# Kernel optimization log

Hardware: AMD Instinct MI355X
Metric: run time of the kernel (lower is better)

## Reference

```python
import jax, jax.numpy as jnp
import numpy as np

B, S, H = 64, 4096, 512

def setup_inputs() -> dict:
    key = jax.random.key(0)
    ks = jax.random.split(key, 8)
    decoder_output = jax.random.normal(ks[0], (B, H), dtype=jnp.float32)
    encoder_output = jax.random.normal(ks[1], (B, S, 2 * H), dtype=jnp.float32)
    mask = jax.random.randint(ks[2], (B, S), 0, 2).astype(bool)
    mask = mask.at[:, 0].set(True)  # guarantee at least one valid position per row
    sc_h = 1.0 / np.sqrt(2 * H)
    sc_s = 1.0 / np.sqrt(H)
    W_h_w = jax.random.uniform(ks[3], (H, 2 * H), jnp.float32, -sc_h, sc_h)
    W_h_b = jax.random.uniform(ks[4], (H,), jnp.float32, -sc_h, sc_h)
    W_s_w = jax.random.uniform(ks[5], (H, H), jnp.float32, -sc_s, sc_s)
    W_s_b = jax.random.uniform(ks[6], (H,), jnp.float32, -sc_s, sc_s)
    v_w = jax.random.uniform(ks[7], (1, H), jnp.float32, -sc_s, sc_s)
    return {"decoder_output": decoder_output, "encoder_output": encoder_output,
            "mask": mask, "W_h_w": W_h_w, "W_h_b": W_h_b,
            "W_s_w": W_s_w, "W_s_b": W_s_b, "v_w": v_w}

def reference(decoder_output, encoder_output, mask, W_h_w, W_h_b, W_s_w, W_s_b, v_w):
    # enc proj: [B,S,H]; dec proj: [B,H] broadcast over S
    enc = jnp.einsum('bse,he->bsh', encoder_output, W_h_w) + W_h_b
    dec = decoder_output @ W_s_w.T + W_s_b  # [B,H]
    x = jnp.tanh(enc + dec[:, None, :])     # [B,S,H]
    scores = jnp.einsum('bsh,h->bs', x, v_w[0])  # [B,S]
    masked = jnp.where(mask, scores, -jnp.inf)
    return jax.nn.softmax(masked, axis=-1)
```

## Files before the change

### kernel.cpp

```cpp
#include <hip/hip_runtime.h>
#include <math.h>

typedef __attribute__((ext_vector_type(8))) short bf16x8;
typedef __attribute__((ext_vector_type(4))) float f32x4;
typedef __attribute__((ext_vector_type(4))) unsigned short u16x4;

#define NB 64
#define NS 4096
#define NH 512
#define NE 1024
#define APITCH 80

__device__ __forceinline__ unsigned short f2bf(float f) {
  unsigned int u = __float_as_uint(f);
  u += 0x7fffu + ((u >> 16) & 1u);
  return (unsigned short)(u >> 16);
}

__device__ __forceinline__ float fast_tanh(float x) {
  float e = __expf(2.0f * x);
  return 1.0f - 2.0f * __builtin_amdgcn_rcpf(e + 1.0f);
}

__global__ __launch_bounds__(256) void prep_b_kernel(const float* __restrict__ W,
                                                     unsigned short* __restrict__ Bp) {
  const int t = blockIdx.x * 256 + threadIdx.x;
  const int lane = t & 63;
  const int ni = (t >> 6) & 3;
  const int kb = (t >> 8) & 31;
  const int w = t >> 13;
  const int col = w * 64 + ni * 16 + (lane & 15);
  const int k0 = kb * 32 + (lane >> 4) * 8;
  const float* src = W + col * NE + k0;
  float4 a = *(const float4*)src;
  float4 b = *(const float4*)(src + 4);
  union { bf16x8 v; unsigned short u[8]; } p;
  p.u[0] = f2bf(a.x); p.u[1] = f2bf(a.y); p.u[2] = f2bf(a.z); p.u[3] = f2bf(a.w);
  p.u[4] = f2bf(b.x); p.u[5] = f2bf(b.y); p.u[6] = f2bf(b.z); p.u[7] = f2bf(b.w);
  *(bf16x8*)(Bp + (long long)t * 8) = p.v;
}

__global__ __launch_bounds__(512) void prep_dec_kernel(const float* __restrict__ dec,
                                                       const float* __restrict__ Wsw,
                                                       const float* __restrict__ Wsb,
                                                       const float* __restrict__ Whb,
                                                       float* __restrict__ decb) {
  int b = blockIdx.x;
  int h = threadIdx.x;
  const float4* dr = (const float4*)(dec + b * NH);
  const float4* wr = (const float4*)(Wsw + h * NH);
  float sum = Wsb[h] + Whb[h];
#pragma unroll 8
  for (int i = 0; i < NH / 4; ++i) {
    float4 a = dr[i], w = wr[i];
    sum += a.x * w.x + a.y * w.y + a.z * w.z + a.w * w.w;
  }
  decb[b * NH + h] = sum;
}

__global__ __launch_bounds__(512, 4) void fused_main(const float* __restrict__ enc,
                                                     const unsigned short* __restrict__ Bp,
                                                     const float* __restrict__ decb,
                                                     const float* __restrict__ vw,
                                                     float* __restrict__ scores) {
  __shared__ __align__(16) char As[2][64 * APITCH];
  __shared__ float ssc[64];

  const int tid = threadIdx.x;
  const int lane = tid & 63;
  const int wave = tid >> 6;
  const int r15 = lane & 15;
  const int c4 = lane >> 4;
  const long long m0 = (long long)blockIdx.x * 64;

  if (tid < 64) ssc[tid] = 0.0f;

  const int arow = tid >> 3;
  const int achk = tid & 7;
  const float* aload = enc + (m0 + arow) * NE + achk * 4;
  const int awr = arow * APITCH + achk * 8;

  const unsigned short* const bb = Bp + (long long)wave * 32 * 2048 + lane * 8;

  f32x4 acc[4][4];
#pragma unroll
  for (int mi = 0; mi < 4; ++mi)
#pragma unroll
    for (int ni = 0; ni < 4; ++ni) {
      f32x4 z = {0.f, 0.f, 0.f, 0.f};
      acc[mi][ni] = z;
    }

  bf16x8 bcur[4];
#pragma unroll
  for (int ni = 0; ni < 4; ++ni) bcur[ni] = *(const bf16x8*)(bb + ni * 512);
  {
    float4 a0 = *(const float4*)(aload);
    unsigned int p0, p1;
    asm("v_cvt_pk_bf16_f32 %0, %1, %2" : "=v"(p0) : "v"(a0.x), "v"(a0.y));
    asm("v_cvt_pk_bf16_f32 %0, %1, %2" : "=v"(p1) : "v"(a0.z), "v"(a0.w));
    uint2 wv; wv.x = p0; wv.y = p1;
    *(uint2*)(&As[0][0] + awr) = wv;
  }
  float4 aCur = *(const float4*)(aload + 32);
  asm volatile("s_waitcnt lgkmcnt(0)" ::: "memory");
  __builtin_amdgcn_s_barrier();
  __builtin_amdgcn_sched_barrier(0);

#pragma unroll
  for (int t = 0; t < 32; ++t) {
    const char* Ab = &As[t & 1][0];
    float4 aNew;
    if (t < 30) aNew = *(const float4*)(aload + (t + 2) * 32);
    bf16x8 af[4];
#pragma unroll
    for (int mi = 0; mi < 4; ++mi)
      af[mi] = *(const bf16x8*)(Ab + (mi * 16 + r15) * APITCH + c4 * 16);
    __builtin_amdgcn_s_setprio(1);
#pragma unroll
    for (int mi = 0; mi < 4; ++mi)
#pragma unroll
      for (int ni = 0; ni < 4; ++ni)
        acc[mi][ni] = __builtin_amdgcn_mfma_f32_16x16x32_bf16(af[mi], bcur[ni],
                                                              acc[mi][ni], 0, 0, 0);
    __builtin_amdgcn_s_setprio(0);
    if (t < 31) {
      const bf16x8* bp = (const bf16x8*)(bb + (t + 1) * 2048);
#pragma unroll
      for (int ni = 0; ni < 4; ++ni) bcur[ni] = bp[ni * 64];
    }
    if (t < 31) {
      unsigned int p0, p1;
      asm("v_cvt_pk_bf16_f32 %0, %1, %2" : "=v"(p0) : "v"(aCur.x), "v"(aCur.y));
      asm("v_cvt_pk_bf16_f32 %0, %1, %2" : "=v"(p1) : "v"(aCur.z), "v"(aCur.w));
      uint2 wv; wv.x = p0; wv.y = p1;
      *(uint2*)(&As[(t & 1) ^ 1][0] + awr) = wv;
      aCur = aNew;
    }
    asm volatile("s_waitcnt lgkmcnt(0)" ::: "memory");
    __builtin_amdgcn_sched_barrier(0);
    __builtin_amdgcn_s_barrier();
  }

  const int bidx = (int)(m0 >> 12);
  const float* decrow = decb + bidx * NH;
  float part[4][4];
#pragma unroll
  for (int mi = 0; mi < 4; ++mi)
#pragma unroll
    for (int j = 0; j < 4; ++j) part[mi][j] = 0.f;

#pragma unroll
  for (int ni = 0; ni < 4; ++ni) {
    int col = (wave << 6) + ni * 16 + r15;
    float vc = vw[col];
    float dc = decrow[col];
#pragma unroll
    for (int mi = 0; mi < 4; ++mi)
#pragma unroll
      for (int j = 0; j < 4; ++j)
        part[mi][j] += vc * fast_tanh(acc[mi][ni][j] + dc);
  }
#pragma unroll
  for (int off = 1; off < 16; off <<= 1)
#pragma unroll
    for (int mi = 0; mi < 4; ++mi)
#pragma unroll
      for (int j = 0; j < 4; ++j)
        part[mi][j] += __shfl_xor(part[mi][j], off, 64);

  if (r15 == 0) {
#pragma unroll
    for (int mi = 0; mi < 4; ++mi)
#pragma unroll
      for (int j = 0; j < 4; ++j)
        atomicAdd(&ssc[mi * 16 + c4 * 4 + j], part[mi][j]);
  }
  __syncthreads();
  if (tid < 64) scores[m0 + tid] = ssc[tid];
}

__global__ __launch_bounds__(1024) void softmax_kernel(const float* __restrict__ scores,
                                                       const int* __restrict__ mask,
                                                       float* __restrict__ out) {
  __shared__ float rmax[16];
  __shared__ float rsum[16];
  const int b = blockIdx.x;
  const int t = threadIdx.x;
  const int wid = t >> 6;
  const int ln = t & 63;
  const int base = b * NS;

  float s[4];
  int mk[4];
  float mx = -INFINITY;
#pragma unroll
  for (int i = 0; i < 4; ++i) {
    int idx = t + i * 1024;
    s[i] = scores[base + idx];
    mk[i] = mask[base + idx];
    if (mk[i]) mx = fmaxf(mx, s[i]);
  }
#pragma unroll
  for (int off = 1; off < 64; off <<= 1) mx = fmaxf(mx, __shfl_xor(mx, off, 64));
  if (ln == 0) rmax[wid] = mx;
  __syncthreads();
  float m2 = -INFINITY;
#pragma unroll
  for (int i = 0; i < 16; ++i) m2 = fmaxf(m2, rmax[i]);

  float e[4];
  float sum = 0.f;
#pragma unroll
  for (int i = 0; i < 4; ++i) {
    e[i] = mk[i] ? expf(s[i] - m2) : 0.f;
    sum += e[i];
  }
#pragma unroll
  for (int off = 1; off < 64; off <<= 1) sum += __shfl_xor(sum, off, 64);
  if (ln == 0) rsum[wid] = sum;
  __syncthreads();
  float tot = 0.f;
#pragma unroll
  for (int i = 0; i < 16; ++i) tot += rsum[i];
  float inv = 1.0f / tot;
#pragma unroll
  for (int i = 0; i < 4; ++i) {
    int idx = t + i * 1024;
    out[base + idx] = e[i] * inv;
  }
}

extern "C" void kernel_launch(void* const* d_in, const int* in_sizes, int n_in,
                              void* d_out, int out_size, void* d_ws, size_t ws_size,
                              hipStream_t stream) {
  const float* dec = (const float*)d_in[0];
  const float* enc = (const float*)d_in[1];
  const int* mask = (const int*)d_in[2];
  const float* Whw = (const float*)d_in[3];
  const float* Whb = (const float*)d_in[4];
  const float* Wsw = (const float*)d_in[5];
  const float* Wsb = (const float*)d_in[6];
  const float* vw = (const float*)d_in[7];
  float* out = (float*)d_out;

  unsigned short* Bp = (unsigned short*)d_ws;
  float* decb = (float*)((char*)d_ws + (1 << 20));
  float* scoresb = (float*)((char*)d_ws + (1 << 20) + (128 << 10));

  prep_b_kernel<<<dim3(256), dim3(256), 0, stream>>>(Whw, Bp);
  prep_dec_kernel<<<dim3(64), dim3(512), 0, stream>>>(dec, Wsw, Wsb, Whb, decb);
  fused_main<<<dim3(4096), dim3(512), 0, stream>>>(enc, Bp, decb, vw, scoresb);
  softmax_kernel<<<dim3(64), dim3(1024), 0, stream>>>(scoresb, mask, out);
}
```

Baseline: 385.1 us.

## Double-buffer B fragments and split each k-step into four barrier-separated phases

```diff
diff --git a/kernel.cpp b/kernel.cpp
--- a/kernel.cpp
+++ b/kernel.cpp
@@ -91,9 +91,9 @@
       acc[mi][ni] = z;
     }
 
-  bf16x8 bcur[4];
-#pragma unroll
-  for (int ni = 0; ni < 4; ++ni) bcur[ni] = *(const bf16x8*)(bb + ni * 512);
+  bf16x8 bA[4], bB[4];
+#pragma unroll
+  for (int ni = 0; ni < 4; ++ni) bA[ni] = *(const bf16x8*)(bb + ni * 512);
   {
     float4 a0 = *(const float4*)(aload);
     unsigned int p0, p1;
@@ -110,36 +110,36 @@
 #pragma unroll
   for (int t = 0; t < 32; ++t) {
     const char* Ab = &As[t & 1][0];
+    const bf16x8* bpn = (const bf16x8*)(bb + (t + 1) * 2048);
     float4 aNew;
-    if (t < 30) aNew = *(const float4*)(aload + (t + 2) * 32);
-    bf16x8 af[4];
-#pragma unroll
-    for (int mi = 0; mi < 4; ++mi)
-      af[mi] = *(const bf16x8*)(Ab + (mi * 16 + r15) * APITCH + c4 * 16);
-    __builtin_amdgcn_s_setprio(1);
-#pragma unroll
-    for (int mi = 0; mi < 4; ++mi)
+#pragma unroll
+    for (int p = 0; p < 4; ++p) {
+      if (p == 0 && t < 30) aNew = *(const float4*)(aload + (t + 2) * 32);
+      if (t < 31) {
+        if (t & 1) bA[p] = bpn[p * 64];
+        else       bB[p] = bpn[p * 64];
+      }
+      bf16x8 af = *(const bf16x8*)(Ab + (p * 16 + r15) * APITCH + c4 * 16);
+      __builtin_amdgcn_s_setprio(1);
 #pragma unroll
       for (int ni = 0; ni < 4; ++ni)
-        acc[mi][ni] = __builtin_amdgcn_mfma_f32_16x16x32_bf16(af[mi], bcur[ni],
-                                                              acc[mi][ni], 0, 0, 0);
-    __builtin_amdgcn_s_setprio(0);
-    if (t < 31) {
-      const bf16x8* bp = (const bf16x8*)(bb + (t + 1) * 2048);
-#pragma unroll
-      for (int ni = 0; ni < 4; ++ni) bcur[ni] = bp[ni * 64];
+        acc[p][ni] = __builtin_amdgcn_mfma_f32_16x16x32_bf16(
+            af, (t & 1) ? bB[ni] : bA[ni], acc[p][ni], 0, 0, 0);
+      __builtin_amdgcn_s_setprio(0);
+      if (p == 3) {
+        if (t < 31) {
+          unsigned int w0, w1;
+          asm("v_cvt_pk_bf16_f32 %0, %1, %2" : "=v"(w0) : "v"(aCur.x), "v"(aCur.y));
+          asm("v_cvt_pk_bf16_f32 %0, %1, %2" : "=v"(w1) : "v"(aCur.z), "v"(aCur.w));
+          uint2 wv; wv.x = w0; wv.y = w1;
+          *(uint2*)(&As[(t & 1) ^ 1][0] + awr) = wv;
+          aCur = aNew;
+        }
+        asm volatile("s_waitcnt lgkmcnt(0)" ::: "memory");
+        __builtin_amdgcn_sched_barrier(0);
+      }
+      __builtin_amdgcn_s_barrier();
     }
-    if (t < 31) {
-      unsigned int p0, p1;
-      asm("v_cvt_pk_bf16_f32 %0, %1, %2" : "=v"(p0) : "v"(aCur.x), "v"(aCur.y));
-      asm("v_cvt_pk_bf16_f32 %0, %1, %2" : "=v"(p1) : "v"(aCur.z), "v"(aCur.w));
-      uint2 wv; wv.x = p0; wv.y = p1;
-      *(uint2*)(&As[(t & 1) ^ 1][0] + awr) = wv;
-      aCur = aNew;
-    }
-    asm volatile("s_waitcnt lgkmcnt(0)" ::: "memory");
-    __builtin_amdgcn_sched_barrier(0);
-    __builtin_amdgcn_s_barrier();
   }
 
   const int bidx = (int)(m0 >> 12);
```

Measured after the change: 394.2 us. 2.4% more time.

## Deepen A-tile pipeline to four LDS buffers and prefetch fragments during MFMAs

Applied to the files above, without the earlier changes.

```diff
diff --git a/kernel.cpp b/kernel.cpp
--- a/kernel.cpp
+++ b/kernel.cpp
@@ -63,7 +63,7 @@
                                                      const float* __restrict__ decb,
                                                      const float* __restrict__ vw,
                                                      float* __restrict__ scores) {
-  __shared__ __align__(16) char As[2][64 * APITCH];
+  __shared__ __align__(16) char As[4][64 * APITCH];
   __shared__ float ssc[64];
 
   const int tid = threadIdx.x;
@@ -79,6 +79,7 @@
   const int achk = tid & 7;
   const float* aload = enc + (m0 + arow) * NE + achk * 4;
   const int awr = arow * APITCH + achk * 8;
+  const int rdb = r15 * APITCH + c4 * 16;
 
   const unsigned short* const bb = Bp + (long long)wave * 32 * 2048 + lane * 8;
 
@@ -95,51 +96,73 @@
 #pragma unroll
   for (int ni = 0; ni < 4; ++ni) bcur[ni] = *(const bf16x8*)(bb + ni * 512);
   {
-    float4 a0 = *(const float4*)(aload);
-    unsigned int p0, p1;
-    asm("v_cvt_pk_bf16_f32 %0, %1, %2" : "=v"(p0) : "v"(a0.x), "v"(a0.y));
-    asm("v_cvt_pk_bf16_f32 %0, %1, %2" : "=v"(p1) : "v"(a0.z), "v"(a0.w));
-    uint2 wv; wv.x = p0; wv.y = p1;
-    *(uint2*)(&As[0][0] + awr) = wv;
-  }
-  float4 aCur = *(const float4*)(aload + 32);
+    float4 p0 = *(const float4*)(aload);
+    float4 p1 = *(const float4*)(aload + 32);
+    unsigned int w0, w1;
+    asm("v_cvt_pk_bf16_f32 %0, %1, %2" : "=v"(w0) : "v"(p0.x), "v"(p0.y));
+    asm("v_cvt_pk_bf16_f32 %0, %1, %2" : "=v"(w1) : "v"(p0.z), "v"(p0.w));
+    uint2 wv0; wv0.x = w0; wv0.y = w1;
+    *(uint2*)(&As[0][0] + awr) = wv0;
+    asm("v_cvt_pk_bf16_f32 %0, %1, %2" : "=v"(w0) : "v"(p1.x), "v"(p1.y));
+    asm("v_cvt_pk_bf16_f32 %0, %1, %2" : "=v"(w1) : "v"(p1.z), "v"(p1.w));
+    uint2 wv1; wv1.x = w0; wv1.y = w1;
+    *(uint2*)(&As[1][0] + awr) = wv1;
+  }
+  float4 slotE = *(const float4*)(aload + 64);
+  float4 slotO;
   asm volatile("s_waitcnt lgkmcnt(0)" ::: "memory");
   __builtin_amdgcn_s_barrier();
-  __builtin_amdgcn_sched_barrier(0);
+
+  bf16x8 af[4];
+#pragma unroll
+  for (int mi = 0; mi < 4; ++mi)
+    af[mi] = *(const bf16x8*)(&As[0][0] + mi * 16 * APITCH + rdb);
 
 #pragma unroll
   for (int t = 0; t < 32; ++t) {
-    const char* Ab = &As[t & 1][0];
-    float4 aNew;
-    if (t < 30) aNew = *(const float4*)(aload + (t + 2) * 32);
-    bf16x8 af[4];
-#pragma unroll
-    for (int mi = 0; mi < 4; ++mi)
-      af[mi] = *(const bf16x8*)(Ab + (mi * 16 + r15) * APITCH + c4 * 16);
+    if (t < 29) {
+      if (t & 1) slotE = *(const float4*)(aload + (t + 3) * 32);
+      else       slotO = *(const float4*)(aload + (t + 3) * 32);
+    }
+    const char* Abn = &As[(t + 1) & 3][0];
+    bf16x8 afn0, afn1, afn2, afn3;
+    if (t < 31) afn0 = *(const bf16x8*)(Abn + rdb);
     __builtin_amdgcn_s_setprio(1);
 #pragma unroll
-    for (int mi = 0; mi < 4; ++mi)
-#pragma unroll
-      for (int ni = 0; ni < 4; ++ni)
-        acc[mi][ni] = __builtin_amdgcn_mfma_f32_16x16x32_bf16(af[mi], bcur[ni],
-                                                              acc[mi][ni], 0, 0, 0);
+    for (int ni = 0; ni < 4; ++ni)
+      acc[0][ni] = __builtin_amdgcn_mfma_f32_16x16x32_bf16(af[0], bcur[ni], acc[0][ni], 0, 0, 0);
+    if (t < 31) afn1 = *(const bf16x8*)(Abn + 1280 + rdb);
+#pragma unroll
+    for (int ni = 0; ni < 4; ++ni)
+      acc[1][ni] = __builtin_amdgcn_mfma_f32_16x16x32_bf16(af[1], bcur[ni], acc[1][ni], 0, 0, 0);
+    if (t < 31) afn2 = *(const bf16x8*)(Abn + 2560 + rdb);
+#pragma unroll
+    for (int ni = 0; ni < 4; ++ni)
+      acc[2][ni] = __builtin_amdgcn_mfma_f32_16x16x32_bf16(af[2], bcur[ni], acc[2][ni], 0, 0, 0);
+    if (t < 31) afn3 = *(const bf16x8*)(Abn + 3840 + rdb);
+#pragma unroll
+    for (int ni = 0; ni < 4; ++ni)
+      acc[3][ni] = __builtin_amdgcn_mfma_f32_16x16x32_bf16(af[3], bcur[ni], acc[3][ni], 0, 0, 0);
     __builtin_amdgcn_s_setprio(0);
     if (t < 31) {
       const bf16x8* bp = (const bf16x8*)(bb + (t + 1) * 2048);
 #pragma unroll
       for (int ni = 0; ni < 4; ++ni) bcur[ni] = bp[ni * 64];
     }
+    if (t < 30) {
+      float4 s = (t & 1) ? slotO : slotE;
+      unsigned int w0, w1;
+      asm("v_cvt_pk_bf16_f32 %0, %1, %2" : "=v"(w0) : "v"(s.x), "v"(s.y));
+      asm("v_cvt_pk_bf16_f32 %0, %1, %2" : "=v"(w1) : "v"(s.z), "v"(s.w));
+      uint2 wv; wv.x = w0; wv.y = w1;
+      *(uint2*)(&As[(t + 2) & 3][0] + awr) = wv;
+    }
     if (t < 31) {
-      unsigned int p0, p1;
-      asm("v_cvt_pk_bf16_f32 %0, %1, %2" : "=v"(p0) : "v"(aCur.x), "v"(aCur.y));
-      asm("v_cvt_pk_bf16_f32 %0, %1, %2" : "=v"(p1) : "v"(aCur.z), "v"(aCur.w));
-      uint2 wv; wv.x = p0; wv.y = p1;
-      *(uint2*)(&As[(t & 1) ^ 1][0] + awr) = wv;
-      aCur = aNew;
-    }
-    asm volatile("s_waitcnt lgkmcnt(0)" ::: "memory");
-    __builtin_amdgcn_sched_barrier(0);
-    __builtin_amdgcn_s_barrier();
+      af[0] = afn0; af[1] = afn1; af[2] = afn2; af[3] = afn3;
+      asm volatile("s_waitcnt lgkmcnt(0)" ::: "memory");
+      __builtin_amdgcn_sched_barrier(0);
+      __builtin_amdgcn_s_barrier();
+    }
   }
 
   const int bidx = (int)(m0 >> 12);
```

Result: no change. 386.7 us (+0.4%).
